# Optimization experiments

Hardware: AMD Instinct MI355X
Metric: run time of the kernel (lower is better)

## Reference

```python
import jax, jax.numpy as jnp
import numpy as np

D_MODEL = 1024
NUM_HEADS = 16
D_K = D_MODEL // NUM_HEADS
B, T = 2, 2048


def setup_inputs() -> dict:
    key = jax.random.key(0)
    ks = jax.random.split(key, 11)
    s = 1.0 / np.sqrt(D_MODEL)
    inp = {
        "q": jax.random.normal(ks[0], (B, T, D_MODEL), jnp.float32),
        "k": jax.random.normal(ks[1], (B, T, D_MODEL), jnp.float32),
        "v": jax.random.normal(ks[2], (B, T, D_MODEL), jnp.float32),
        "mask": jnp.tril(jnp.ones((1, 1, T, T), jnp.int32)),  # causal
        "wq": jax.random.normal(ks[3], (D_MODEL, D_MODEL), jnp.float32) * s,
        "bq": jnp.zeros((D_MODEL,), jnp.float32),
        "wk": jax.random.normal(ks[4], (D_MODEL, D_MODEL), jnp.float32) * s,
        "bk": jnp.zeros((D_MODEL,), jnp.float32),
        "wv": jax.random.normal(ks[5], (D_MODEL, D_MODEL), jnp.float32) * s,
        "bv": jnp.zeros((D_MODEL,), jnp.float32),
        "wo": jax.random.normal(ks[6], (D_MODEL, D_MODEL), jnp.float32) * s,
        "bo": jnp.zeros((D_MODEL,), jnp.float32),
    }
    return inp


def reference(q, k, v, mask, wq, bq, wk, bk, wv, bv, wo, bo):
    Bq, Tq, _ = q.shape
    Tk = k.shape[1]
    # projections, split into heads: (B, H, T, d_k)
    qh = (q @ wq + bq).reshape(Bq, Tq, NUM_HEADS, D_K).transpose(0, 2, 1, 3)
    kh = (k @ wk + bk).reshape(Bq, Tk, NUM_HEADS, D_K).transpose(0, 2, 1, 3)
    vh = (v @ wv + bv).reshape(Bq, Tk, NUM_HEADS, D_K).transpose(0, 2, 1, 3)
    scores = jnp.einsum("bhqd,bhkd->bhqk", qh, kh) / jnp.sqrt(jnp.float32(D_K))
    scores = jnp.where(mask == 0, jnp.float32(-1e9), scores)
    attn = jax.nn.softmax(scores, axis=-1)
    ctx = jnp.einsum("bhqk,bhkd->bhqd", attn, vh)
    ctx = ctx.transpose(0, 2, 1, 3).reshape(Bq, Tq, D_MODEL)
    return ctx @ wo + bo
```

## Files before the change

kernel.cpp:

```cpp
#include <hip/hip_runtime.h>
#include <hip/hip_bf16.h>

#define DM 1024
#define NH 16
#define DK 64
#define TT 2048
#define BATCH 2

typedef __attribute__((ext_vector_type(8))) short bf16x8;
typedef __attribute__((ext_vector_type(4))) float f32x4;
typedef unsigned short u16;

__device__ inline u16 f2b(float x){ __hip_bfloat16 h = __float2bfloat16(x); return *reinterpret_cast<u16*>(&h); }

__device__ inline void gl_lds16(const u16* g, u16* l) {
  __builtin_amdgcn_global_load_lds(
      (const __attribute__((address_space(1))) unsigned int*)g,
      (__attribute__((address_space(3))) unsigned int*)l, 16, 0, 0);
}

__global__ __launch_bounds__(256) void cvt3(const float* __restrict__ q, const float* __restrict__ k,
                                            const float* __restrict__ v, u16* __restrict__ qb,
                                            u16* __restrict__ kb, u16* __restrict__ vb) {
  const float* src = blockIdx.z==0 ? q : blockIdx.z==1 ? k : v;
  u16* dst = blockIdx.z==0 ? qb : blockIdx.z==1 ? kb : vb;
  size_t i = ((size_t)blockIdx.x*256 + threadIdx.x)*8;
  f32x4 a = *(const f32x4*)(src+i);
  f32x4 b = *(const f32x4*)(src+i+4);
  union { bf16x8 v8; u16 e[8]; } u;
  #pragma unroll
  for (int j=0;j<4;j++){ u.e[j] = f2b(a[j]); u.e[4+j] = f2b(b[j]); }
  *(bf16x8*)(dst+i) = u.v8;
}

__global__ void transposecvt4(const float* __restrict__ wq, const float* __restrict__ wk,
                              const float* __restrict__ wv, const float* __restrict__ wo,
                              u16* __restrict__ wt) {
  __shared__ float tile[32][33];
  const float* src = blockIdx.z==0 ? wq : blockIdx.z==1 ? wk : blockIdx.z==2 ? wv : wo;
  u16* dst = wt + (size_t)blockIdx.z*DM*DM;
  int x  = blockIdx.x*32 + threadIdx.x;
  int y0 = blockIdx.y*32 + threadIdx.y;
  #pragma unroll
  for (int i=0;i<32;i+=8) tile[threadIdx.y+i][threadIdx.x] = src[(size_t)(y0+i)*DM + x];
  __syncthreads();
  int xo = blockIdx.y*32 + threadIdx.x;
  int yo = blockIdx.x*32 + threadIdx.y;
  #pragma unroll
  for (int i=0;i<32;i+=8) dst[(size_t)(yo+i)*DM + xo] = f2b(tile[threadIdx.x][threadIdx.y+i]);
}

__device__ __forceinline__ void gemm_body(const u16* __restrict__ A, const u16* __restrict__ W,
                                          const float* __restrict__ bias, void* __restrict__ outv,
                                          int mode, float oscale) {
  __shared__ u16 As[128*32];
  __shared__ u16 Bs[128*32];
  const int tid = threadIdx.x, lane = tid & 63, wid = tid >> 6;
  const int li = lane & 15, quad = lane >> 4;
  const int row0 = blockIdx.x*128, col0 = blockIdx.y*128;
  const int wr = wid & 1, wc = wid >> 1;

  f32x4 acc[4][4];
  #pragma unroll
  for (int i=0;i<4;i++)
    #pragma unroll
    for (int j=0;j<4;j++) acc[i][j] = f32x4{0.f,0.f,0.f,0.f};

  const int srow = lane >> 2;
  const int scol = (lane & 3) * 8;

  for (int k0 = 0; k0 < DM; k0 += 32) {
    #pragma unroll
    for (int c = 0; c < 2; c++) {
      int ch = wid*2 + c;
      gl_lds16(A + (size_t)(row0 + ch*16 + srow)*DM + k0 + scol, As + ch*512);
      gl_lds16(W + (size_t)(col0 + ch*16 + srow)*DM + k0 + scol, Bs + ch*512);
    }
    __syncthreads();
    bf16x8 a[4], b[4];
    #pragma unroll
    for (int i=0;i<4;i++) a[i] = *(const bf16x8*)&As[(wr*64 + i*16 + li)*32 + quad*8];
    #pragma unroll
    for (int j=0;j<4;j++) b[j] = *(const bf16x8*)&Bs[(wc*64 + j*16 + li)*32 + quad*8];
    #pragma unroll
    for (int i=0;i<4;i++)
      #pragma unroll
      for (int j=0;j<4;j++)
        acc[i][j] = __builtin_amdgcn_mfma_f32_16x16x32_bf16(a[i], b[j], acc[i][j], 0,0,0);
    __syncthreads();
  }

  #pragma unroll
  for (int j=0;j<4;j++) {
    int col = col0 + wc*64 + j*16 + li;
    float bsv = bias[col];
    #pragma unroll
    for (int i=0;i<4;i++) {
      #pragma unroll
      for (int r=0;r<4;r++) {
        int row = row0 + wr*64 + i*16 + quad*4 + r;
        float v = (acc[i][j][r] + bsv) * oscale;
        if (mode == 2) {
          ((float*)outv)[(size_t)row*DM + col] = v;
        } else {
          int bb = row >> 11, t = row & (TT-1);
          int hh = col >> 6,  d = col & 63;
          size_t idx = (mode == 0)
            ? ((((size_t)(bb*NH + hh)*TT + t) << 6) + d)
            : ((((size_t)(bb*NH + hh)*DK + d)*TT) + t);
          ((u16*)outv)[idx] = f2b(v);
        }
      }
    }
  }
}

__global__ __launch_bounds__(256) void gemm_qkv(const u16* __restrict__ qb, const u16* __restrict__ kb,
                                                const u16* __restrict__ vb, const u16* __restrict__ wt,
                                                const float* __restrict__ bq, const float* __restrict__ bk,
                                                const float* __restrict__ bv,
                                                u16* __restrict__ qh, u16* __restrict__ kh,
                                                u16* __restrict__ vhT) {
  int z = blockIdx.z;
  const u16* A = z==0 ? qb : z==1 ? kb : vb;
  const u16* W = wt + (size_t)z*DM*DM;
  const float* bias = z==0 ? bq : z==1 ? bk : bv;
  u16* out = z==0 ? qh : z==1 ? kh : vhT;
  gemm_body(A, W, bias, out, z==2 ? 1 : 0, z==0 ? 0.125f : 1.0f);
}

__global__ __launch_bounds__(256) void gemm_out(const u16* __restrict__ ctx, const u16* __restrict__ wt,
                                                const float* __restrict__ bo, float* __restrict__ out) {
  gemm_body(ctx, wt, bo, out, 2, 1.0f);
}

__global__ __launch_bounds__(256) void flash(const u16* __restrict__ qh, const u16* __restrict__ kh,
                                             const u16* __restrict__ vhT, u16* __restrict__ ctx) {
  const int bh = blockIdx.x;
  const int qt = gridDim.y - 1 - blockIdx.y;
  const int b = bh >> 4, h = bh & 15;
  const u16* Q  = qh  + (size_t)bh*TT*DK;
  const u16* K  = kh  + (size_t)bh*TT*DK;
  const u16* Vt = vhT + (size_t)bh*DK*TT;

  const int tid = threadIdx.x, lane = tid & 63, wid = tid >> 6;
  const int li = lane & 15, quad = lane >> 4;

  __shared__ u16 Kl[64][72];
  __shared__ u16 Vl[64][72];
  __shared__ u16 Pb[4][2][16][72];

  const int qrow0 = qt*128 + wid*16;
  bf16x8 qf[2][2];
  #pragma unroll
  for (int m=0;m<2;m++){
    qf[m][0] = *(const bf16x8*)&Q[(size_t)(qrow0+m*64+li)*DK +      quad*8];
    qf[m][1] = *(const bf16x8*)&Q[(size_t)(qrow0+m*64+li)*DK + 32 + quad*8];
  }

  f32x4 o[2][4];
  float lp[2][4];
  #pragma unroll
  for (int m=0;m<2;m++){
    #pragma unroll
    for (int d=0;d<4;d++) o[m][d] = f32x4{0.f,0.f,0.f,0.f};
    #pragma unroll
    for (int r=0;r<4;r++) lp[m][r] = 0.f;
  }

  const int sr = tid >> 3;
  const int sc = (tid & 7) * 8;
  const int itmax = 2*qt + 1;

  bf16x8 kr0 = *(const bf16x8*)&K[(size_t)(sr   )*DK + sc];
  bf16x8 kr1 = *(const bf16x8*)&K[(size_t)(sr+32)*DK + sc];
  bf16x8 vr0 = *(const bf16x8*)&Vt[(size_t)(sr   )*TT + sc];
  bf16x8 vr1 = *(const bf16x8*)&Vt[(size_t)(sr+32)*TT + sc];

  for (int it = 0; it <= itmax; it++) {
    const int k0 = it*64;
    __syncthreads();
    *(bf16x8*)&Kl[sr   ][sc] = kr0;
    *(bf16x8*)&Kl[sr+32][sc] = kr1;
    *(bf16x8*)&Vl[sr   ][sc] = vr0;
    *(bf16x8*)&Vl[sr+32][sc] = vr1;
    __syncthreads();
    if (it < itmax) {
      const int k1 = k0 + 64;
      kr0 = *(const bf16x8*)&K[(size_t)(k1+sr   )*DK + sc];
      kr1 = *(const bf16x8*)&K[(size_t)(k1+sr+32)*DK + sc];
      vr0 = *(const bf16x8*)&Vt[(size_t)(sr   )*TT + k1 + sc];
      vr1 = *(const bf16x8*)&Vt[(size_t)(sr+32)*TT + k1 + sc];
    }

    #pragma unroll
    for (int m=0;m<2;m++) {
      if (m==0 && it==itmax) continue;
      const bool maskme = (m==0) ? (it==itmax-1) : (it==itmax);

      f32x4 s[4];
      #pragma unroll
      for (int c=0;c<4;c++) {
        bf16x8 kf0 = *(const bf16x8*)&Kl[c*16+li][     quad*8];
        bf16x8 kf1 = *(const bf16x8*)&Kl[c*16+li][32 + quad*8];
        f32x4 t = __builtin_amdgcn_mfma_f32_16x16x32_bf16(qf[m][0], kf0, f32x4{0.f,0.f,0.f,0.f}, 0,0,0);
        s[c]    = __builtin_amdgcn_mfma_f32_16x16x32_bf16(qf[m][1], kf1, t, 0,0,0);
      }
      float p[4][4];
      if (maskme) {
        #pragma unroll
        for (int c=0;c<4;c++){
          int col = k0 + c*16 + li;
          #pragma unroll
          for (int r=0;r<4;r++){
            int row = qrow0 + m*64 + quad*4 + r;
            p[c][r] = (col <= row) ? __expf(s[c][r]) : 0.f;
          }
        }
      } else {
        #pragma unroll
        for (int c=0;c<4;c++)
          #pragma unroll
          for (int r=0;r<4;r++)
            p[c][r] = __expf(s[c][r]);
      }
      #pragma unroll
      for (int c=0;c<4;c++)
        #pragma unroll
        for (int r=0;r<4;r++)
          lp[m][r] += p[c][r];

      #pragma unroll
      for (int c=0;c<4;c++)
        #pragma unroll
        for (int r=0;r<4;r++)
          Pb[wid][m][quad*4+r][c*16+li] = f2b(p[c][r]);
      __builtin_amdgcn_wave_barrier();
      __asm__ __volatile__("s_waitcnt lgkmcnt(0)");
      bf16x8 pf0 = *(const bf16x8*)&Pb[wid][m][li][     quad*8];
      bf16x8 pf1 = *(const bf16x8*)&Pb[wid][m][li][32 + quad*8];

      #pragma unroll
      for (int d=0;d<4;d++){
        bf16x8 vf0 = *(const bf16x8*)&Vl[d*16+li][     quad*8];
        bf16x8 vf1 = *(const bf16x8*)&Vl[d*16+li][32 + quad*8];
        o[m][d] = __builtin_amdgcn_mfma_f32_16x16x32_bf16(pf0, vf0, o[m][d], 0,0,0);
        o[m][d] = __builtin_amdgcn_mfma_f32_16x16x32_bf16(pf1, vf1, o[m][d], 0,0,0);
      }
    }
  }

  #pragma unroll
  for (int m=0;m<2;m++)
    #pragma unroll
    for (int r=0;r<4;r++){
      float x = lp[m][r];
      #pragma unroll
      for (int off=1; off<16; off<<=1) x += __shfl_xor(x, off, 64);
      lp[m][r] = x;
    }

  #pragma unroll
  for (int m=0;m<2;m++)
    #pragma unroll
    for (int d=0;d<4;d++)
      #pragma unroll
      for (int r=0;r<4;r++){
        int row = qrow0 + m*64 + quad*4 + r;
        float v = o[m][d][r] / lp[m][r];
        ctx[(size_t)(b*TT + row)*DM + h*DK + d*16 + li] = f2b(v);
      }
}

extern "C" void kernel_launch(void* const* d_in, const int* in_sizes, int n_in,
                              void* d_out, int out_size, void* d_ws, size_t ws_size,
                              hipStream_t stream) {
  const float* q   = (const float*)d_in[0];
  const float* k   = (const float*)d_in[1];
  const float* v   = (const float*)d_in[2];
  const float* wq  = (const float*)d_in[4];
  const float* bq  = (const float*)d_in[5];
  const float* wk  = (const float*)d_in[6];
  const float* bk  = (const float*)d_in[7];
  const float* wv  = (const float*)d_in[8];
  const float* bv  = (const float*)d_in[9];
  const float* wo  = (const float*)d_in[10];
  const float* bo  = (const float*)d_in[11];
  float* out = (float*)d_out;

  const size_t SZ = (size_t)BATCH*TT*DM;
  u16* wt  = (u16*)d_ws;
  u16* qb  = wt + (size_t)4*DM*DM;
  u16* kb  = qb + SZ;
  u16* vb  = kb + SZ;
  u16* qh  = vb + SZ;
  u16* kh  = qh + SZ;
  u16* vhT = kh + SZ;
  u16* ctx = qb;

  cvt3<<<dim3((int)(SZ/2048), 1, 3), 256, 0, stream>>>(q, k, v, qb, kb, vb);
  transposecvt4<<<dim3(32,32,4), dim3(32,8,1), 0, stream>>>(wq, wk, wv, wo, wt);

  gemm_qkv<<<dim3(4096/128, DM/128, 3), 256, 0, stream>>>(qb, kb, vb, wt, bq, bk, bv, qh, kh, vhT);

  flash<<<dim3(BATCH*NH, TT/128), 256, 0, stream>>>(qh, kh, vhT, ctx);

  gemm_out<<<dim3(4096/128, DM/128, 1), 256, 0, stream>>>(ctx, wt + (size_t)3*DM*DM, bo, out);
}
```

Baseline: 249.7 us.

## Merge prep kernels, balance causal flash via paired tiles, narrow out-GEMM tiles

Merges the input-conversion and weight-transpose kernels into one launch. Restructures flash attention so each block handles two 64-row query tiles (pr and 31-pr), giving every block equal causal work. It also swaps the MFMA operand order to get transposed score and output fragments, which allows vectorized P and ctx stores. Splits the output projection into a dedicated 128x64-tile GEMM to double the block count. This adds complexity: a serial two-phase loop per block and a prep grid with idle blocks.

```diff
diff --git a/kernel.cpp b/kernel.cpp
--- a/kernel.cpp
+++ b/kernel.cpp
@@ -9,6 +9,7 @@
 
 typedef __attribute__((ext_vector_type(8))) short bf16x8;
 typedef __attribute__((ext_vector_type(4))) float f32x4;
+typedef __attribute__((ext_vector_type(4))) unsigned short u16x4;
 typedef unsigned short u16;
 
 __device__ inline u16 f2b(float x){ __hip_bfloat16 h = __float2bfloat16(x); return *reinterpret_cast<u16*>(&h); }
@@ -19,39 +20,45 @@
       (__attribute__((address_space(3))) unsigned int*)l, 16, 0, 0);
 }
 
-__global__ __launch_bounds__(256) void cvt3(const float* __restrict__ q, const float* __restrict__ k,
-                                            const float* __restrict__ v, u16* __restrict__ qb,
-                                            u16* __restrict__ kb, u16* __restrict__ vb) {
-  const float* src = blockIdx.z==0 ? q : blockIdx.z==1 ? k : v;
-  u16* dst = blockIdx.z==0 ? qb : blockIdx.z==1 ? kb : vb;
-  size_t i = ((size_t)blockIdx.x*256 + threadIdx.x)*8;
-  f32x4 a = *(const f32x4*)(src+i);
-  f32x4 b = *(const f32x4*)(src+i+4);
-  union { bf16x8 v8; u16 e[8]; } u;
-  #pragma unroll
-  for (int j=0;j<4;j++){ u.e[j] = f2b(a[j]); u.e[4+j] = f2b(b[j]); }
-  *(bf16x8*)(dst+i) = u.v8;
-}
-
-__global__ void transposecvt4(const float* __restrict__ wq, const float* __restrict__ wk,
-                              const float* __restrict__ wv, const float* __restrict__ wo,
-                              u16* __restrict__ wt) {
-  __shared__ float tile[32][33];
-  const float* src = blockIdx.z==0 ? wq : blockIdx.z==1 ? wk : blockIdx.z==2 ? wv : wo;
-  u16* dst = wt + (size_t)blockIdx.z*DM*DM;
-  int x  = blockIdx.x*32 + threadIdx.x;
-  int y0 = blockIdx.y*32 + threadIdx.y;
-  #pragma unroll
-  for (int i=0;i<32;i+=8) tile[threadIdx.y+i][threadIdx.x] = src[(size_t)(y0+i)*DM + x];
-  __syncthreads();
-  int xo = blockIdx.y*32 + threadIdx.x;
-  int yo = blockIdx.x*32 + threadIdx.y;
-  #pragma unroll
-  for (int i=0;i<32;i+=8) dst[(size_t)(yo+i)*DM + xo] = f2b(tile[threadIdx.x][threadIdx.y+i]);
+__global__ __launch_bounds__(256) void prep(const float* __restrict__ q, const float* __restrict__ k,
+                                            const float* __restrict__ v,
+                                            const float* __restrict__ wq, const float* __restrict__ wk,
+                                            const float* __restrict__ wv, const float* __restrict__ wo,
+                                            u16* __restrict__ qb, u16* __restrict__ kb,
+                                            u16* __restrict__ vb, u16* __restrict__ wt) {
+  int z = blockIdx.z;
+  if (z < 3) {
+    const float* src = z==0 ? q : z==1 ? k : v;
+    u16* dst = z==0 ? qb : z==1 ? kb : vb;
+    size_t i = ((size_t)blockIdx.x*256 + threadIdx.x)*8;
+    f32x4 a = *(const f32x4*)(src+i);
+    f32x4 b = *(const f32x4*)(src+i+4);
+    union { bf16x8 v8; u16 e[8]; } u;
+    #pragma unroll
+    for (int j=0;j<4;j++){ u.e[j] = f2b(a[j]); u.e[4+j] = f2b(b[j]); }
+    *(bf16x8*)(dst+i) = u.v8;
+  } else {
+    int bx = blockIdx.x;
+    if (bx >= 1024) return;
+    __shared__ float tile[32][33];
+    const float* src = z==3 ? wq : z==4 ? wk : z==5 ? wv : wo;
+    u16* dst = wt + (size_t)(z-3)*DM*DM;
+    int bxx = bx & 31, byy = bx >> 5;
+    int tx = threadIdx.x & 31, ty = threadIdx.x >> 5;
+    int x  = bxx*32 + tx;
+    int y0 = byy*32 + ty;
+    #pragma unroll
+    for (int i=0;i<32;i+=8) tile[ty+i][tx] = src[(size_t)(y0+i)*DM + x];
+    __syncthreads();
+    int xo = byy*32 + tx;
+    int yo = bxx*32 + ty;
+    #pragma unroll
+    for (int i=0;i<32;i+=8) dst[(size_t)(yo+i)*DM + xo] = f2b(tile[tx][ty+i]);
+  }
 }
 
 __device__ __forceinline__ void gemm_body(const u16* __restrict__ A, const u16* __restrict__ W,
-                                          const float* __restrict__ bias, void* __restrict__ outv,
+                                          const float* __restrict__ bias, u16* __restrict__ outv,
                                           int mode, float oscale) {
   __shared__ u16 As[128*32];
   __shared__ u16 Bs[128*32];
@@ -100,16 +107,12 @@
       for (int r=0;r<4;r++) {
         int row = row0 + wr*64 + i*16 + quad*4 + r;
         float v = (acc[i][j][r] + bsv) * oscale;
-        if (mode == 2) {
-          ((float*)outv)[(size_t)row*DM + col] = v;
-        } else {
-          int bb = row >> 11, t = row & (TT-1);
-          int hh = col >> 6,  d = col & 63;
-          size_t idx = (mode == 0)
-            ? ((((size_t)(bb*NH + hh)*TT + t) << 6) + d)
-            : ((((size_t)(bb*NH + hh)*DK + d)*TT) + t);
-          ((u16*)outv)[idx] = f2b(v);
-        }
+        int bb = row >> 11, t = row & (TT-1);
+        int hh = col >> 6,  d = col & 63;
+        size_t idx = (mode == 0)
+          ? ((((size_t)(bb*NH + hh)*TT + t) << 6) + d)
+          : ((((size_t)(bb*NH + hh)*DK + d)*TT) + t);
+        outv[idx] = f2b(v);
       }
     }
   }
@@ -129,15 +132,64 @@
   gemm_body(A, W, bias, out, z==2 ? 1 : 0, z==0 ? 0.125f : 1.0f);
 }
 
-__global__ __launch_bounds__(256) void gemm_out(const u16* __restrict__ ctx, const u16* __restrict__ wt,
-                                                const float* __restrict__ bo, float* __restrict__ out) {
-  gemm_body(ctx, wt, bo, out, 2, 1.0f);
+__global__ __launch_bounds__(256) void gemm_out64(const u16* __restrict__ A, const u16* __restrict__ W,
+                                                  const float* __restrict__ bias, float* __restrict__ out) {
+  __shared__ u16 As[128*32];
+  __shared__ u16 Bs[64*32];
+  const int tid = threadIdx.x, lane = tid & 63, wid = tid >> 6;
+  const int li = lane & 15, quad = lane >> 4;
+  const int row0 = blockIdx.x*128, col0 = blockIdx.y*64;
+  const int wr = wid & 1, wc = wid >> 1;
+
+  f32x4 acc[4][2];
+  #pragma unroll
+  for (int i=0;i<4;i++)
+    #pragma unroll
+    for (int j=0;j<2;j++) acc[i][j] = f32x4{0.f,0.f,0.f,0.f};
+
+  const int srow = lane >> 2;
+  const int scol = (lane & 3) * 8;
+
+  for (int k0 = 0; k0 < DM; k0 += 32) {
+    #pragma unroll
+    for (int c = 0; c < 2; c++) {
+      int ch = wid*2 + c;
+      gl_lds16(A + (size_t)(row0 + ch*16 + srow)*DM + k0 + scol, As + ch*512);
+    }
+    gl_lds16(W + (size_t)(col0 + wid*16 + srow)*DM + k0 + scol, Bs + wid*512);
+    __syncthreads();
+    bf16x8 a[4], b[2];
+    #pragma unroll
+    for (int i=0;i<4;i++) a[i] = *(const bf16x8*)&As[(wr*64 + i*16 + li)*32 + quad*8];
+    #pragma unroll
+    for (int j=0;j<2;j++) b[j] = *(const bf16x8*)&Bs[(wc*32 + j*16 + li)*32 + quad*8];
+    #pragma unroll
+    for (int i=0;i<4;i++)
+      #pragma unroll
+      for (int j=0;j<2;j++)
+        acc[i][j] = __builtin_amdgcn_mfma_f32_16x16x32_bf16(a[i], b[j], acc[i][j], 0,0,0);
+    __syncthreads();
+  }
+
+  #pragma unroll
+  for (int j=0;j<2;j++) {
+    int col = col0 + wc*32 + j*16 + li;
+    float bsv = bias[col];
+    #pragma unroll
+    for (int i=0;i<4;i++) {
+      #pragma unroll
+      for (int r=0;r<4;r++) {
+        int row = row0 + wr*64 + i*16 + quad*4 + r;
+        out[(size_t)row*DM + col] = acc[i][j][r] + bsv;
+      }
+    }
+  }
 }
 
 __global__ __launch_bounds__(256) void flash(const u16* __restrict__ qh, const u16* __restrict__ kh,
                                              const u16* __restrict__ vhT, u16* __restrict__ ctx) {
   const int bh = blockIdx.x;
-  const int qt = gridDim.y - 1 - blockIdx.y;
+  const int pr = blockIdx.y;
   const int b = bh >> 4, h = bh & 15;
   const u16* Q  = qh  + (size_t)bh*TT*DK;
   const u16* K  = kh  + (size_t)bh*TT*DK;
@@ -148,75 +200,70 @@
 
   __shared__ u16 Kl[64][72];
   __shared__ u16 Vl[64][72];
-  __shared__ u16 Pb[4][2][16][72];
-
-  const int qrow0 = qt*128 + wid*16;
-  bf16x8 qf[2][2];
-  #pragma unroll
-  for (int m=0;m<2;m++){
-    qf[m][0] = *(const bf16x8*)&Q[(size_t)(qrow0+m*64+li)*DK +      quad*8];
-    qf[m][1] = *(const bf16x8*)&Q[(size_t)(qrow0+m*64+li)*DK + 32 + quad*8];
-  }
-
-  f32x4 o[2][4];
-  float lp[2][4];
-  #pragma unroll
-  for (int m=0;m<2;m++){
-    #pragma unroll
-    for (int d=0;d<4;d++) o[m][d] = f32x4{0.f,0.f,0.f,0.f};
-    #pragma unroll
-    for (int r=0;r<4;r++) lp[m][r] = 0.f;
-  }
+  __shared__ u16 Pb[4][16][72];
 
   const int sr = tid >> 3;
   const int sc = (tid & 7) * 8;
-  const int itmax = 2*qt + 1;
 
   bf16x8 kr0 = *(const bf16x8*)&K[(size_t)(sr   )*DK + sc];
   bf16x8 kr1 = *(const bf16x8*)&K[(size_t)(sr+32)*DK + sc];
   bf16x8 vr0 = *(const bf16x8*)&Vt[(size_t)(sr   )*TT + sc];
   bf16x8 vr1 = *(const bf16x8*)&Vt[(size_t)(sr+32)*TT + sc];
 
-  for (int it = 0; it <= itmax; it++) {
-    const int k0 = it*64;
-    __syncthreads();
-    *(bf16x8*)&Kl[sr   ][sc] = kr0;
-    *(bf16x8*)&Kl[sr+32][sc] = kr1;
-    *(bf16x8*)&Vl[sr   ][sc] = vr0;
-    *(bf16x8*)&Vl[sr+32][sc] = vr1;
-    __syncthreads();
-    if (it < itmax) {
-      const int k1 = k0 + 64;
-      kr0 = *(const bf16x8*)&K[(size_t)(k1+sr   )*DK + sc];
-      kr1 = *(const bf16x8*)&K[(size_t)(k1+sr+32)*DK + sc];
-      vr0 = *(const bf16x8*)&Vt[(size_t)(sr   )*TT + k1 + sc];
-      vr1 = *(const bf16x8*)&Vt[(size_t)(sr+32)*TT + k1 + sc];
-    }
-
-    #pragma unroll
-    for (int m=0;m<2;m++) {
-      if (m==0 && it==itmax) continue;
-      const bool maskme = (m==0) ? (it==itmax-1) : (it==itmax);
+  #pragma unroll
+  for (int ph = 0; ph < 2; ph++) {
+    const int qt = (ph == 0) ? pr : (31 - pr);
+    const int nt = qt + 1;
+    const int qrow0 = qt*64 + wid*16;
+
+    bf16x8 qf0 = *(const bf16x8*)&Q[(size_t)(qrow0+li)*DK +      quad*8];
+    bf16x8 qf1 = *(const bf16x8*)&Q[(size_t)(qrow0+li)*DK + 32 + quad*8];
+
+    f32x4 o[4];
+    #pragma unroll
+    for (int d=0;d<4;d++) o[d] = f32x4{0.f,0.f,0.f,0.f};
+    float lp = 0.f;
+
+    for (int it = 0; it < nt; it++) {
+      const int k0 = it*64;
+      __syncthreads();
+      *(bf16x8*)&Kl[sr   ][sc] = kr0;
+      *(bf16x8*)&Kl[sr+32][sc] = kr1;
+      *(bf16x8*)&Vl[sr   ][sc] = vr0;
+      *(bf16x8*)&Vl[sr+32][sc] = vr1;
+      __syncthreads();
+      if (it+1 < nt) {
+        const int k1 = k0 + 64;
+        kr0 = *(const bf16x8*)&K[(size_t)(k1+sr   )*DK + sc];
+        kr1 = *(const bf16x8*)&K[(size_t)(k1+sr+32)*DK + sc];
+        vr0 = *(const bf16x8*)&Vt[(size_t)(sr   )*TT + k1 + sc];
+        vr1 = *(const bf16x8*)&Vt[(size_t)(sr+32)*TT + k1 + sc];
+      } else if (ph == 0) {
+        kr0 = *(const bf16x8*)&K[(size_t)(sr   )*DK + sc];
+        kr1 = *(const bf16x8*)&K[(size_t)(sr+32)*DK + sc];
+        vr0 = *(const bf16x8*)&Vt[(size_t)(sr   )*TT + sc];
+        vr1 = *(const bf16x8*)&Vt[(size_t)(sr+32)*TT + sc];
+      }
 
       f32x4 s[4];
       #pragma unroll
       for (int c=0;c<4;c++) {
         bf16x8 kf0 = *(const bf16x8*)&Kl[c*16+li][     quad*8];
         bf16x8 kf1 = *(const bf16x8*)&Kl[c*16+li][32 + quad*8];
-        f32x4 t = __builtin_amdgcn_mfma_f32_16x16x32_bf16(qf[m][0], kf0, f32x4{0.f,0.f,0.f,0.f}, 0,0,0);
-        s[c]    = __builtin_amdgcn_mfma_f32_16x16x32_bf16(qf[m][1], kf1, t, 0,0,0);
-      }
+        f32x4 t = __builtin_amdgcn_mfma_f32_16x16x32_bf16(kf0, qf0, f32x4{0.f,0.f,0.f,0.f}, 0,0,0);
+        s[c]    = __builtin_amdgcn_mfma_f32_16x16x32_bf16(kf1, qf1, t, 0,0,0);
+      }
+      const bool dg = (it == nt-1);
+      const int qq = qrow0 + li;
       float p[4][4];
-      if (maskme) {
+      if (dg) {
         #pragma unroll
-        for (int c=0;c<4;c++){
-          int col = k0 + c*16 + li;
+        for (int c=0;c<4;c++)
           #pragma unroll
           for (int r=0;r<4;r++){
-            int row = qrow0 + m*64 + quad*4 + r;
-            p[c][r] = (col <= row) ? __expf(s[c][r]) : 0.f;
+            int key = k0 + c*16 + quad*4 + r;
+            p[c][r] = (key <= qq) ? __expf(s[c][r]) : 0.f;
           }
-        }
       } else {
         #pragma unroll
         for (int c=0;c<4;c++)
@@ -228,48 +275,42 @@
       for (int c=0;c<4;c++)
         #pragma unroll
         for (int r=0;r<4;r++)
-          lp[m][r] += p[c][r];
-
-      #pragma unroll
-      for (int c=0;c<4;c++)
+          lp += p[c][r];
+
+      #pragma unroll
+      for (int c=0;c<4;c++) {
+        u16x4 w;
         #pragma unroll
-        for (int r=0;r<4;r++)
-          Pb[wid][m][quad*4+r][c*16+li] = f2b(p[c][r]);
+        for (int r=0;r<4;r++) w[r] = f2b(p[c][r]);
+        *(u16x4*)&Pb[wid][li][c*16 + quad*4] = w;
+      }
       __builtin_amdgcn_wave_barrier();
       __asm__ __volatile__("s_waitcnt lgkmcnt(0)");
-      bf16x8 pf0 = *(const bf16x8*)&Pb[wid][m][li][     quad*8];
-      bf16x8 pf1 = *(const bf16x8*)&Pb[wid][m][li][32 + quad*8];
+      bf16x8 pf0 = *(const bf16x8*)&Pb[wid][li][     quad*8];
+      bf16x8 pf1 = *(const bf16x8*)&Pb[wid][li][32 + quad*8];
 
       #pragma unroll
       for (int d=0;d<4;d++){
         bf16x8 vf0 = *(const bf16x8*)&Vl[d*16+li][     quad*8];
         bf16x8 vf1 = *(const bf16x8*)&Vl[d*16+li][32 + quad*8];
-        o[m][d] = __builtin_amdgcn_mfma_f32_16x16x32_bf16(pf0, vf0, o[m][d], 0,0,0);
-        o[m][d] = __builtin_amdgcn_mfma_f32_16x16x32_bf16(pf1, vf1, o[m][d], 0,0,0);
-      }
-    }
-  }
-
-  #pragma unroll
-  for (int m=0;m<2;m++)
-    #pragma unroll
-    for (int r=0;r<4;r++){
-      float x = lp[m][r];
-      #pragma unroll
-      for (int off=1; off<16; off<<=1) x += __shfl_xor(x, off, 64);
-      lp[m][r] = x;
-    }
-
-  #pragma unroll
-  for (int m=0;m<2;m++)
-    #pragma unroll
-    for (int d=0;d<4;d++)
-      #pragma unroll
-      for (int r=0;r<4;r++){
-        int row = qrow0 + m*64 + quad*4 + r;
-        float v = o[m][d][r] / lp[m][r];
-        ctx[(size_t)(b*TT + row)*DM + h*DK + d*16 + li] = f2b(v);
-      }
+        o[d] = __builtin_amdgcn_mfma_f32_16x16x32_bf16(vf0, pf0, o[d], 0,0,0);
+        o[d] = __builtin_amdgcn_mfma_f32_16x16x32_bf16(vf1, pf1, o[d], 0,0,0);
+      }
+    }
+
+    lp += __shfl_xor(lp, 16, 64);
+    lp += __shfl_xor(lp, 32, 64);
+    float rl = 1.0f / lp;
+
+    const int qq = qrow0 + li;
+    #pragma unroll
+    for (int d=0;d<4;d++){
+      u16x4 w;
+      #pragma unroll
+      for (int r=0;r<4;r++) w[r] = f2b(o[d][r] * rl);
+      *(u16x4*)&ctx[(size_t)(b*TT + qq)*DM + h*DK + d*16 + quad*4] = w;
+    }
+  }
 }
 
 extern "C" void kernel_launch(void* const* d_in, const int* in_sizes, int n_in,
@@ -298,12 +339,11 @@
   u16* vhT = kh + SZ;
   u16* ctx = qb;
 
-  cvt3<<<dim3((int)(SZ/2048), 1, 3), 256, 0, stream>>>(q, k, v, qb, kb, vb);
-  transposecvt4<<<dim3(32,32,4), dim3(32,8,1), 0, stream>>>(wq, wk, wv, wo, wt);
+  prep<<<dim3(2048, 1, 7), 256, 0, stream>>>(q, k, v, wq, wk, wv, wo, qb, kb, vb, wt);
 
   gemm_qkv<<<dim3(4096/128, DM/128, 3), 256, 0, stream>>>(qb, kb, vb, wt, bq, bk, bv, qh, kh, vhT);
 
-  flash<<<dim3(BATCH*NH, TT/128), 256, 0, stream>>>(qh, kh, vhT, ctx);
-
-  gemm_out<<<dim3(4096/128, DM/128, 1), 256, 0, stream>>>(ctx, wt + (size_t)3*DM*DM, bo, out);
-}
+  flash<<<dim3(BATCH*NH, 16), 256, 0, stream>>>(qh, kh, vhT, ctx);
+
+  gemm_out64<<<dim3(4096/128, DM/64), 256, 0, stream>>>(ctx, wt + (size_t)3*DM*DM, bo, out);
+}
```

After: 245.5 us. No clear change (-1.7%).
